# Kernel optimization log

Measured on AMD Instinct MI355X. Metric: run time of the kernel, lower is better.

The kernel has to match this reference:

```python
import jax, jax.numpy as jnp
import numpy as np

B, C, OC, K, HW = 32, 256, 256, 3, 56
M, G = 2, 2
GAP = max(16, C // 16)          # input_gap = 16
MO = M * OC                      # fc1 out channels = 512
FC2_OUT = OC * C * K * K         # 589824
PER = FC2_OUT // MO              # per-group out channels of fc2 = 1152


def setup_inputs() -> dict:
    key = jax.random.key(0)
    ks = jax.random.split(key, 6)
    x = jax.random.normal(ks[0], (B, C, HW, HW), dtype=jnp.float32)
    reduce_w = jax.random.normal(ks[1], (GAP, C), dtype=jnp.float32) / np.sqrt(C)
    reduce_b = jnp.zeros((GAP,), dtype=jnp.float32)
    fc1_w = jax.random.normal(ks[2], (MO, GAP), dtype=jnp.float32) / np.sqrt(GAP)
    # fc2: grouped 1x1 conv, groups=G*OC=512, 1 in-channel per group -> weight (FC2_OUT,)
    fc2_w = jax.random.normal(ks[3], (FC2_OUT,), dtype=jnp.float32)
    fc2_b = jax.random.normal(ks[4], (FC2_OUT,), dtype=jnp.float32) * 0.01
    return {"x": x, "reduce_w": reduce_w, "reduce_b": reduce_b,
            "fc1_w": fc1_w, "fc2_w": fc2_w, "fc2_b": fc2_b}


def reference(x, reduce_w, reduce_b, fc1_w, fc2_w, fc2_b):
    b, c, h, w = x.shape
    # global average pool -> (b, C)
    gap = x.mean(axis=(2, 3))
    # reduce: 1x1 conv on 1x1 map == linear
    g = gap @ reduce_w.T + reduce_b                      # (b, GAP)
    # fc1 (no bias) + sigmoid
    a = jax.nn.sigmoid(g @ fc1_w.T)                      # (b, MO)
    # fc2: grouped 1x1 conv with 1 input channel per group:
    # out[:, g*PER + j] = a[:, g] * fc2_w[g*PER + j] + fc2_b[g*PER + j]
    wk = a[:, :, None] * fc2_w.reshape(MO, PER)[None] + fc2_b.reshape(MO, PER)[None]
    wk = wk.reshape(b * OC, c, K, K)                     # per-sample conv kernels
    pad = K // 2
    y = jax.lax.conv_general_dilated(
        x.reshape(1, b * c, h, w), wk,
        window_strides=(1, 1), padding=[(pad, pad), (pad, pad)],
        feature_group_count=b,
        dimension_numbers=("NCHW", "OIHW", "NCHW"))
    return y.reshape(b, OC, y.shape[2], y.shape[3])
```

## Files before the change

### kernel.cpp

```cpp
#include <hip/hip_runtime.h>
#include <hip/hip_bf16.h>
#include <stdint.h>

#define NB   32
#define NC   256
#define NOC  256
#define HWD  56
#define NPIX 3136
#define PW   58
#define PPIX 3364
#define KTOT 2304
#define MOD  512
#define GAPD 16

#define XBT_BYTES ((size_t)NB * PPIX * NC * 2)
#define WA_BYTES  ((size_t)NB * NOC * KTOT * 2)

typedef __bf16 bf16x8 __attribute__((ext_vector_type(8)));
typedef float  f32x4  __attribute__((ext_vector_type(4)));
typedef unsigned short u16x8 __attribute__((ext_vector_type(8)));

__device__ __forceinline__ unsigned short f2bf(float f) {
    union { float f; unsigned int u; } v; v.f = f;
    unsigned int u = v.u;
    return (unsigned short)((u + 0x7FFFu + ((u >> 16) & 1u)) >> 16);
}

__global__ void wk_kernel(const float* __restrict__ gap,
                          const float* __restrict__ rw, const float* __restrict__ rb,
                          const float* __restrict__ f1w,
                          const float* __restrict__ f2w, const float* __restrict__ f2b,
                          unsigned short* __restrict__ wa) {
    __shared__ float sgap[NB * 257];
    __shared__ float srw[GAPD * 257];
    __shared__ float ssg[NB * GAPD];
    __shared__ float sa[2 * NB];
    __shared__ float sw[KTOT];
    __shared__ float sbv[KTOT];
    int oc = blockIdx.x, c = threadIdx.x;
    #pragma unroll
    for (int i = 0; i < 32; ++i) {
        int idx = i * 256 + c;
        sgap[(idx >> 8) * 257 + (idx & 255)] = gap[idx];
    }
    #pragma unroll
    for (int i = 0; i < 16; ++i) {
        int idx = i * 256 + c;
        srw[(idx >> 8) * 257 + (idx & 255)] = rw[idx];
    }
    const float4* wsrc = (const float4*)(f2w + (size_t)oc * KTOT);
    const float4* bsrc = (const float4*)(f2b + (size_t)oc * KTOT);
    #pragma unroll
    for (int i = 0; i < 3; ++i) {
        int idx = i * 256 + c;
        if (idx < 576) {
            ((float4*)sw)[idx] = wsrc[idx];
            ((float4*)sbv)[idx] = bsrc[idx];
        }
    }
    __syncthreads();
    #pragma unroll
    for (int e = 0; e < 2; ++e) {
        int pair = c * 2 + e;
        int b = pair >> 4, tt = pair & 15;
        float s = rb[tt];
        for (int k = 0; k < NC; ++k) s += sgap[b * 257 + k] * srw[tt * 257 + k];
        ssg[b * GAPD + tt] = s;
    }
    __syncthreads();
    if (c < 64) {
        int b = c >> 1, e = c & 1;
        float s = 0.f;
        #pragma unroll
        for (int tt = 0; tt < GAPD; ++tt)
            s += ssg[b * GAPD + tt] * f1w[(2 * oc + e) * GAPD + tt];
        sa[c] = 1.0f / (1.0f + __expf(-s));
    }
    __syncthreads();
    float w9[9], b9[9];
    #pragma unroll
    for (int s = 0; s < 9; ++s) { w9[s] = sw[c * 9 + s]; b9[s] = sbv[c * 9 + s]; }
    for (int b = 0; b < NB; ++b) {
        float a0 = sa[2 * b], a1 = sa[2 * b + 1];
        unsigned short* dst = wa + (size_t)(b * NOC + oc) * KTOT;
        #pragma unroll
        for (int s = 0; s < 9; ++s) {
            float a = ((c * 9 + s) >= 1152) ? a1 : a0;
            dst[s * NC + c] = f2bf(a * w9[s] + b9[s]);
        }
    }
}

__global__ void halo_kernel(unsigned short* __restrict__ xbt, float* __restrict__ gap) {
    int b = blockIdx.x, t = threadIdx.x;
    gap[b * NC + t] = 0.f;
    unsigned short* xb = xbt + (size_t)b * PPIX * NC;
    u16x8 z = {};
    for (int i = t; i < 3712; i += 256) {
        int r = (i >= 1856) ? 1 : 0;
        int c = i - r * 1856;
        int pix = r * (57 * 58) + (c >> 5);
        *(u16x8*)(xb + (size_t)pix * NC + (c & 31) * 8) = z;
    }
    for (int i = t; i < 3584; i += 256) {
        int row = 1 + (i >> 6);
        int side = (i >> 5) & 1;
        int pix = row * PW + side * 57;
        *(u16x8*)(xb + (size_t)pix * NC + (i & 31) * 8) = z;
    }
}

#define TSTR 59
__global__ void xpose_kernel(const float* __restrict__ x, unsigned short* __restrict__ xbt,
                             float* __restrict__ gap) {
    __shared__ unsigned short tile[NC * TSTR];
    int py = blockIdx.x, b = blockIdx.y, t = threadIdx.x;
    int wv = t >> 6, l = t & 63;
    const float* xs = x + (size_t)b * NC * NPIX + py * HWD;
    int q = l & 15;
    int rb4 = l >> 4;
    #pragma unroll
    for (int it = 0; it < 16; ++it) {
        int c = wv * 64 + it * 4 + rb4;
        float4 v = {0.f, 0.f, 0.f, 0.f};
        if (q < 14) {
            v = *(const float4*)(xs + (size_t)c * NPIX + q * 4);
            unsigned short* tr = tile + c * TSTR + q * 4;
            tr[0] = f2bf(v.x); tr[1] = f2bf(v.y); tr[2] = f2bf(v.z); tr[3] = f2bf(v.w);
        }
        float s4 = v.x + v.y + v.z + v.w;
        s4 += __shfl_xor(s4, 1);
        s4 += __shfl_xor(s4, 2);
        s4 += __shfl_xor(s4, 4);
        s4 += __shfl_xor(s4, 8);
        if (q == 0) atomicAdd(&gap[b * NC + c], s4 * (1.0f / NPIX));
    }
    __syncthreads();
    int cch = t & 31, pg = t >> 5;
    for (int i = 0; i < 7; ++i) {
        int px = pg * 7 + i;
        u16x8 v;
        #pragma unroll
        for (int j = 0; j < 8; ++j) v[j] = tile[(cch * 8 + j) * TSTR + px];
        *(u16x8*)(xbt + ((size_t)b * PPIX + (size_t)(1 + py) * PW + 1 + px) * NC + cch * 8) = v;
    }
}

#define SLICE 32768
#define BOFS  16384

#define PWAIT(N) do { asm volatile("s_waitcnt vmcnt(" #N ")" ::: "memory"); \
    __builtin_amdgcn_s_barrier(); __builtin_amdgcn_sched_barrier(0); } while (0)

__global__ __launch_bounds__(512, 2) void conv_gemm(
    const unsigned short* __restrict__ wa,
    const unsigned short* __restrict__ xbt,
    float* __restrict__ out)
{
    __shared__ __attribute__((aligned(16))) char lds[4 * SLICE];

    const int bid = blockIdx.x;
    const int wg  = (bid & 7) * 56 + (bid >> 3);
    const int b   = wg / 14, nt = wg % 14;

    const int t = threadIdx.x;
    const int w = t >> 6, l = t & 63;
    const int wm = w >> 1, wn = w & 1;

    const unsigned short* waB = wa + (size_t)b * NOC * KTOT;
    const unsigned short* xbB = xbt + (size_t)b * PPIX * NC;

    const unsigned short* srcA[2];
    const unsigned short* srcB[2];
    #pragma unroll
    for (int j = 0; j < 2; ++j) {
        int cix = j * 512 + t;
        int cc  = cix & 63;
        int row = (cix >> 6) * 16 + (cc >> 2);
        int qv  = (cc & 3) ^ ((cc >> 3) & 3);
        srcA[j] = waB + (size_t)row * KTOT + qv * 8;
        int pg = nt * 224 + row; if (pg > NPIX - 1) pg = NPIX - 1;
        int py = pg / 56, px = pg - py * 56;
        srcB[j] = xbB + (size_t)((py + 1) * PW + (px + 1)) * NC + qv * 8;
    }
    const int t16 = t * 16;

    auto issue = [&](int tp, int slot) {
        char* sb = lds + slot * SLICE;
        const int koff = tp * 32;
        const int s9 = tp >> 3;
        const int dy = (s9 >= 6) ? 2 : ((s9 >= 3) ? 1 : 0);
        const int dx = s9 - dy * 3;
        const int bsh = ((dy - 1) * PW + (dx - 1)) * NC + (tp & 7) * 32;
        #pragma unroll
        for (int j = 0; j < 2; ++j)
            __builtin_amdgcn_global_load_lds(
                (const __attribute__((address_space(1))) void*)(srcA[j] + koff),
                (__attribute__((address_space(3))) void*)(sb + j * 8192 + t16), 16, 0, 0);
        #pragma unroll
        for (int j = 0; j < 2; ++j)
            __builtin_amdgcn_global_load_lds(
                (const __attribute__((address_space(1))) void*)(srcB[j] + bsh),
                (__attribute__((address_space(3))) void*)(sb + BOFS + j * 8192 + t16), 16, 0, 0);
    };

    const int physq16 = (((l >> 4) ^ ((l >> 1) & 3)) << 4);
    const int arow = (l & 15) << 6;

    f32x4 acc[4][7] = {};

    auto compute = [&](int slot) {
        const char* sb = lds + slot * SLICE;
        bf16x8 af[4], bfr[7];
        #pragma unroll
        for (int m = 0; m < 4; ++m)
            af[m] = *(const bf16x8*)(sb + (wm * 4 + m) * 1024 + arow + physq16);
        #pragma unroll
        for (int j = 0; j < 7; ++j)
            bfr[j] = *(const bf16x8*)(sb + BOFS + (wn * 7 + j) * 1024 + arow + physq16);
        __builtin_amdgcn_s_setprio(1);
        #pragma unroll
        for (int m = 0; m < 4; ++m)
            #pragma unroll
            for (int j = 0; j < 7; ++j)
                acc[m][j] = __builtin_amdgcn_mfma_f32_16x16x32_bf16(af[m], bfr[j], acc[m][j], 0, 0, 0);
        __builtin_amdgcn_s_setprio(0);
    };

    issue(0, 0); issue(1, 1);

    #pragma unroll 4
    for (int p = 0; p < 70; ++p) {
        issue(p + 2, (p + 2) & 3);
        PWAIT(8);
        compute(p & 3);
    }
    PWAIT(4); compute(70 & 3);
    PWAIT(0); compute(71 & 3);

    const int ocb = wm * 64 + ((l >> 4) << 2);
    const int pxb = nt * 224 + wn * 112 + (l & 15);
    #pragma unroll
    for (int i = 0; i < 4; ++i) {
        #pragma unroll
        for (int j = 0; j < 7; ++j) {
            float* o = out + ((size_t)(b * NOC + ocb + i * 16)) * NPIX + pxb + j * 16;
            o[0]        = acc[i][j][0];
            o[NPIX]     = acc[i][j][1];
            o[2 * NPIX] = acc[i][j][2];
            o[3 * NPIX] = acc[i][j][3];
        }
    }
}

extern "C" void kernel_launch(void* const* d_in, const int* in_sizes, int n_in,
                              void* d_out, int out_size, void* d_ws, size_t ws_size,
                              hipStream_t stream) {
    (void)in_sizes; (void)n_in; (void)out_size; (void)ws_size;
    const float* x   = (const float*)d_in[0];
    const float* rw  = (const float*)d_in[1];
    const float* rb  = (const float*)d_in[2];
    const float* f1w = (const float*)d_in[3];
    const float* f2w = (const float*)d_in[4];
    const float* f2b = (const float*)d_in[5];
    float* out = (float*)d_out;

    char* wsb = (char*)d_ws;
    unsigned short* xbt = (unsigned short*)wsb;
    unsigned short* wa  = (unsigned short*)(wsb + XBT_BYTES);
    float* gap = (float*)(wsb + XBT_BYTES + WA_BYTES);

    halo_kernel<<<dim3(32), 256, 0, stream>>>(xbt, gap);
    xpose_kernel<<<dim3(56, 32), 256, 0, stream>>>(x, xbt, gap);
    wk_kernel<<<dim3(256), 256, 0, stream>>>(gap, rw, rb, f1w, f2w, f2b, wa);
    conv_gemm<<<dim3(448), 512, 0, stream>>>(wa, xbt, out);
}
```

Baseline: 186.1 us.

## Switch conv GEMM to 64-wide K tiles with two-stage LDS double buffering

```diff
diff --git a/kernel.cpp b/kernel.cpp
--- a/kernel.cpp
+++ b/kernel.cpp
@@ -146,8 +146,7 @@
     }
 }
 
-#define SLICE 32768
-#define BOFS  16384
+#define SLICE 65536
 
 #define PWAIT(N) do { asm volatile("s_waitcnt vmcnt(" #N ")" ::: "memory"); \
     __builtin_amdgcn_s_barrier(); __builtin_amdgcn_sched_barrier(0); } while (0)
@@ -157,7 +156,7 @@
     const unsigned short* __restrict__ xbt,
     float* __restrict__ out)
 {
-    __shared__ __attribute__((aligned(16))) char lds[4 * SLICE];
+    __shared__ __attribute__((aligned(16))) char lds[2 * SLICE];
 
     const int bid = blockIdx.x;
     const int wg  = (bid & 7) * 56 + (bid >> 3);
@@ -185,23 +184,27 @@
     }
     const int t16 = t * 16;
 
-    auto issue = [&](int tp, int slot) {
+    auto issue = [&](int kt, int slot) {
         char* sb = lds + slot * SLICE;
-        const int koff = tp * 32;
-        const int s9 = tp >> 3;
+        const int s9 = kt >> 2;
         const int dy = (s9 >= 6) ? 2 : ((s9 >= 3) ? 1 : 0);
         const int dx = s9 - dy * 3;
-        const int bsh = ((dy - 1) * PW + (dx - 1)) * NC + (tp & 7) * 32;
-        #pragma unroll
-        for (int j = 0; j < 2; ++j)
-            __builtin_amdgcn_global_load_lds(
-                (const __attribute__((address_space(1))) void*)(srcA[j] + koff),
-                (__attribute__((address_space(3))) void*)(sb + j * 8192 + t16), 16, 0, 0);
-        #pragma unroll
-        for (int j = 0; j < 2; ++j)
-            __builtin_amdgcn_global_load_lds(
-                (const __attribute__((address_space(1))) void*)(srcB[j] + bsh),
-                (__attribute__((address_space(3))) void*)(sb + BOFS + j * 8192 + t16), 16, 0, 0);
+        const int bsh = ((dy - 1) * PW + (dx - 1)) * NC + (kt & 3) * 64;
+        #pragma unroll
+        for (int h = 0; h < 2; ++h) {
+            #pragma unroll
+            for (int j = 0; j < 2; ++j)
+                __builtin_amdgcn_global_load_lds(
+                    (const __attribute__((address_space(1))) void*)(srcA[j] + kt * 64 + h * 32),
+                    (__attribute__((address_space(3))) void*)(sb + h * 16384 + j * 8192 + t16),
+                    16, 0, 0);
+            #pragma unroll
+            for (int j = 0; j < 2; ++j)
+                __builtin_amdgcn_global_load_lds(
+                    (const __attribute__((address_space(1))) void*)(srcB[j] + bsh + h * 32),
+                    (__attribute__((address_space(3))) void*)(sb + 32768 + h * 16384 + j * 8192 + t16),
+                    16, 0, 0);
+        }
     };
 
     const int physq16 = (((l >> 4) ^ ((l >> 1) & 3)) << 4);
@@ -211,32 +214,38 @@
 
     auto compute = [&](int slot) {
         const char* sb = lds + slot * SLICE;
-        bf16x8 af[4], bfr[7];
-        #pragma unroll
-        for (int m = 0; m < 4; ++m)
-            af[m] = *(const bf16x8*)(sb + (wm * 4 + m) * 1024 + arow + physq16);
-        #pragma unroll
-        for (int j = 0; j < 7; ++j)
-            bfr[j] = *(const bf16x8*)(sb + BOFS + (wn * 7 + j) * 1024 + arow + physq16);
-        __builtin_amdgcn_s_setprio(1);
-        #pragma unroll
-        for (int m = 0; m < 4; ++m)
+        #pragma unroll
+        for (int h = 0; h < 2; ++h) {
+            const char* ab = sb + h * 16384;
+            bf16x8 af[4], bfr[7];
+            #pragma unroll
+            for (int m = 0; m < 4; ++m)
+                af[m] = *(const bf16x8*)(ab + (wm * 4 + m) * 1024 + arow + physq16);
             #pragma unroll
             for (int j = 0; j < 7; ++j)
-                acc[m][j] = __builtin_amdgcn_mfma_f32_16x16x32_bf16(af[m], bfr[j], acc[m][j], 0, 0, 0);
-        __builtin_amdgcn_s_setprio(0);
+                bfr[j] = *(const bf16x8*)(ab + 32768 + (wn * 7 + j) * 1024 + arow + physq16);
+            __builtin_amdgcn_s_setprio(1);
+            #pragma unroll
+            for (int m = 0; m < 4; ++m)
+                #pragma unroll
+                for (int j = 0; j < 7; ++j)
+                    acc[m][j] = __builtin_amdgcn_mfma_f32_16x16x32_bf16(af[m], bfr[j], acc[m][j], 0, 0, 0);
+            __builtin_amdgcn_s_setprio(0);
+        }
     };
 
     issue(0, 0); issue(1, 1);
 
-    #pragma unroll 4
-    for (int p = 0; p < 70; ++p) {
-        issue(p + 2, (p + 2) & 3);
+    #pragma unroll 2
+    for (int p = 0; p < 35; ++p) {
         PWAIT(8);
-        compute(p & 3);
-    }
-    PWAIT(4); compute(70 & 3);
-    PWAIT(0); compute(71 & 3);
+        compute(p & 1);
+        __builtin_amdgcn_s_barrier();
+        __builtin_amdgcn_sched_barrier(0);
+        if (p < 34) issue(p + 2, p & 1);
+    }
+    PWAIT(0);
+    compute(1);
 
     const int ocb = wm * 64 + ((l >> 4) << 2);
     const int pxb = nt * 224 + wn * 112 + (l & 15);
```

After: 206.9 us. +11.2%, slower.
